# Performance work log

Hardware: AMD Instinct MI355X
Metric: run time of the kernel (lower is better)

## Reference

```python
import jax, jax.numpy as jnp
import numpy as np
from jax import lax

N, CIN, COUT, T, V = 32, 64, 128, 256, 25
IC = COUT // 4
EPS = 1e-5


def setup_inputs() -> dict:
    key = jax.random.key(0)
    ks = jax.random.split(key, 16)
    rn = lambda k, shape, s=0.05: jax.random.normal(k, shape, jnp.float32) * s
    inp = {
        'x': jax.random.normal(ks[0], (N, CIN, T, V), jnp.float32),
        'A': rn(ks[1], (V, V), 0.2),
        'w1': rn(ks[2], (IC, CIN)), 'b1': rn(ks[3], (IC,), 0.01),
        'w2': rn(ks[4], (IC, CIN)), 'b2': rn(ks[5], (IC,), 0.01),
        'w3': rn(ks[6], (COUT, CIN)), 'b3': rn(ks[7], (COUT,), 0.01),
        'w4': rn(ks[8], (COUT, CIN)), 'b4': rn(ks[9], (COUT,), 0.01),
        'bn1_g': jnp.ones((COUT,)), 'bn1_b': jnp.zeros((COUT,)),
        'bn1_m': rn(ks[10], (COUT,), 0.1), 'bn1_v': jnp.ones((COUT,)),
        'wt': rn(ks[11], (COUT, COUT, 9, 1)), 'bt': rn(ks[12], (COUT,), 0.01),
        'bn2_g': jnp.ones((COUT,)), 'bn2_b': jnp.zeros((COUT,)),
        'bn2_m': rn(ks[13], (COUT,), 0.1), 'bn2_v': jnp.ones((COUT,)),
        'wr': rn(ks[14], (COUT, CIN)), 'br': rn(ks[15], (COUT,), 0.01),
        'bnr_g': jnp.ones((COUT,)), 'bnr_b': jnp.zeros((COUT,)),
        'bnr_m': jnp.zeros((COUT,)), 'bnr_v': jnp.ones((COUT,)),
    }
    return inp


def _conv1x1(x, w, b):
    # 1x1 Conv2d over (T,V): pure channel mix. x: [N,C,T,V], w: [O,C]
    return jnp.einsum('oc,nctv->notv', w, x) + b[None, :, None, None]


def _bn(x, g, b, m, v):
    # BatchNorm2d in eval mode (running stats)
    scale = g / jnp.sqrt(v + EPS)
    return x * scale[None, :, None, None] + (b - m * scale)[None, :, None, None]


def _forward(x, A, w1, b1, w2, b2, w3, b3, w4, b4,
             bn1_g, bn1_b, bn1_m, bn1_v, wt, bt,
             bn2_g, bn2_b, bn2_m, bn2_v, wr, br,
             bnr_g, bnr_b, bnr_m, bnr_v):
    n, _, t, v = x.shape
    cout = w3.shape[0]
    ic = cout // 4
    x1 = _conv1x1(x, w1, b1).mean(axis=2)  # [N,IC,V]
    x2 = _conv1x1(x, w2, b2).mean(axis=2)  # [N,IC,V]
    a = jax.nn.softmax(x1[..., :, None] - x2[..., None, :], axis=-1)  # [N,IC,V,V]
    x3 = _conv1x1(x, w3, b3).reshape(n, 4, ic, t, v)
    y = jnp.einsum('ncuv,nmctv->nmctu', a, x3).reshape(n, cout, t, v)
    y = y + jnp.einsum('uv,nctv->nctu', A, _conv1x1(x, w4, b4))
    # tcn: BN -> ReLU -> Conv2d (9,1) pad (4,0) -> BN
    y = jax.nn.relu(_bn(y, bn1_g, bn1_b, bn1_m, bn1_v))
    y = lax.conv_general_dilated(
        y, wt, window_strides=(1, 1), padding=[(4, 4), (0, 0)],
        dimension_numbers=('NCHW', 'OIHW', 'NCHW')) + bt[None, :, None, None]
    y = _bn(y, bn2_g, bn2_b, bn2_m, bn2_v)
    # residual branch (in_channels != out_channels): 1x1 conv + BN
    res = _bn(_conv1x1(x, wr, br), bnr_g, bnr_b, bnr_m, bnr_v)
    return jax.nn.relu(y + res)


def reference(x, A, w1, b1, w2, b2, w3, b3, w4, b4,
              bn1_g, bn1_b, bn1_m, bn1_v, wt, bt,
              bn2_g, bn2_b, bn2_m, bn2_v, wr, br,
              bnr_g, bnr_b, bnr_m, bnr_v):
    return _forward(x, A, w1, b1, w2, b2, w3, b3, w4, b4,
                    bn1_g, bn1_b, bn1_m, bn1_v, wt, bt,
                    bn2_g, bn2_b, bn2_m, bn2_v, wr, br,
                    bnr_g, bnr_b, bnr_m, bnr_v)
```

## Files before the change

### kernel.cpp

```cpp
#include <hip/hip_runtime.h>
#include <hip/hip_bf16.h>

typedef unsigned short u16;
typedef unsigned int u32;
typedef unsigned long long u64;
typedef __attribute__((ext_vector_type(8))) short short8;
typedef __attribute__((ext_vector_type(4))) float f32x4;

#define DI __device__ __forceinline__

DI float b2f(u16 v){ u32 u = ((u32)v) << 16; float f; __builtin_memcpy(&f, &u, 4); return f; }
DI u16 f2bu(float f){ __hip_bfloat16 h = __float2bfloat16(f); u16 u; __builtin_memcpy(&u, &h, 2); return u; }

DI void gll16(const u16* g, u16* l){
  __builtin_amdgcn_global_load_lds((const __attribute__((address_space(1))) void*)g,
                                   (__attribute__((address_space(3))) void*)l, 16, 0, 0);
}

__global__ __launch_bounds__(256) void kaux(const float* __restrict__ wt, const float* __restrict__ wrw,
      const float* __restrict__ g2, const float* __restrict__ v2,
      const float* __restrict__ gr, const float* __restrict__ vr,
      const float* __restrict__ w3, const float* __restrict__ w4,
      const float* __restrict__ bt, const float* __restrict__ bb2, const float* __restrict__ m2,
      const float* __restrict__ bbr, const float* __restrict__ mr, const float* __restrict__ brb,
      float* __restrict__ xm, u16* __restrict__ wtb, u16* __restrict__ wrb,
      u16* __restrict__ w3b, u16* __restrict__ w4b,
      float* __restrict__ e0, float* __restrict__ e1, u16* __restrict__ h){
  const int b = blockIdx.x, tid = threadIdx.x;
  if (b < 50){
    const int i = b*1024 + tid*4;
    float4 z = {0.f,0.f,0.f,0.f};
    *(float4*)(xm + i) = z;
  } else if (b < 626){
    const int o = (b-50)*256 + tid;
    const int dt = o >> 14, rem = o & 16383;
    wtb[o] = f2bu(wt[rem*9 + dt]);
  } else if (b < 658){
    const int o = (b-626)*256 + tid;
    const int co = o >> 6;
    const float E0 = g2[co]*rsqrtf(v2[co]+1e-5f);
    const float R0 = gr[co]*rsqrtf(vr[co]+1e-5f);
    wrb[o] = f2bu(wrw[o]*R0/E0);
  } else if (b < 690){
    const int o = (b-658)*256 + tid;
    w3b[o] = f2bu(w3[o]);
  } else if (b < 722){
    const int o = (b-690)*256 + tid;
    w4b[o] = f2bu(w4[o]);
  } else if (b < 786){
    const int j = b - 722, n = j >> 1, side = j & 1;
    short8* base = (short8*)(h + ((size_t)n*6600 + (side ? 6500 : 0))*128);
    short8 z = {0,0,0,0,0,0,0,0};
    for (int i = tid; i < 1600; i += 256) base[i] = z;
  } else {
    if (tid < 128){
      const float scv2 = g2[tid]*rsqrtf(v2[tid]+1e-5f);
      const float scvr = gr[tid]*rsqrtf(vr[tid]+1e-5f);
      e0[tid] = scv2;
      e1[tid] = scv2*bt[tid] + bb2[tid] - m2[tid]*scv2
              + (bbr[tid] - mr[tid]*scvr + scvr*brb[tid]);
    }
  }
}

__global__ __launch_bounds__(256) void kprep2(const float* __restrict__ x, const float* __restrict__ Ab,
                                              u16* __restrict__ xT, u16* __restrict__ xA){
  __shared__ float xl[200*68];
  __shared__ float al[625];
  const int tc = blockIdx.x, n = blockIdx.y, tid = threadIdx.x;
  const int x0t = tc * 200;
  for (int i = tid; i < 625; i += 256) al[i] = Ab[i];
  for (int idx = tid; idx < 12800; idx += 256){
    const int ci = idx / 200, col = idx - ci*200;
    xl[col*68 + ci] = x[((size_t)(n*64+ci))*6400 + x0t + col];
  }
  __syncthreads();
  for (int idx = tid; idx < 3200; idx += 256){
    const int r = idx >> 4, k4 = (idx & 15) << 2;
    const float* src = xl + r*68 + k4;
    u64 pk = (u64)f2bu(src[0]) | ((u64)f2bu(src[1])<<16)
           | ((u64)f2bu(src[2])<<32) | ((u64)f2bu(src[3])<<48);
    *(u64*)(xT + ((size_t)n*6400 + x0t + r)*64 + k4) = pk;
  }
  if (tid < 200){
    const int t_ = tid / 25, u = tid % 25;
    float acc[64];
    #pragma unroll
    for (int k = 0; k < 64; k++) acc[k] = 0.f;
    const float* arow = al + u*25;
    for (int v = 0; v < 25; v++){
      const float a = arow[v];
      const float* xr = xl + (t_*25 + v)*68;
      #pragma unroll
      for (int k = 0; k < 64; k++) acc[k] += a * xr[k];
    }
    u16* dst = xA + ((size_t)n*6400 + x0t + tid)*64;
    #pragma unroll
    for (int k = 0; k < 64; k += 4){
      u64 pk = (u64)f2bu(acc[k]) | ((u64)f2bu(acc[k+1])<<16)
             | ((u64)f2bu(acc[k+2])<<32) | ((u64)f2bu(acc[k+3])<<48);
      *(u64*)(dst + k) = pk;
    }
  }
}

__global__ __launch_bounds__(256) void kmean(const u16* __restrict__ xT, float* __restrict__ xm){
  __shared__ float part[4][1600];
  const int seg = blockIdx.x, n = blockIdx.y, tid = threadIdx.x;
  const int tg = tid>>6, c = tid&63;
  float acc[25];
  #pragma unroll
  for (int v=0;v<25;v++) acc[v]=0.f;
  for (int t = seg*32 + tg; t < seg*32 + 32; t += 4){
    const u16* base = xT + ((size_t)n*6400 + t*25)*64 + c;
    #pragma unroll
    for (int v=0;v<25;v++) acc[v] += b2f(base[v*64]);
  }
  #pragma unroll
  for (int v=0;v<25;v++) part[tg][v*64+c] = acc[v];
  __syncthreads();
  for (int idx = tid; idx < 1600; idx += 256){
    const int v = idx>>6, cc = idx&63;
    const float m = part[0][idx]+part[1][idx]+part[2][idx]+part[3][idx];
    atomicAdd(&xm[(n*64+cc)*25+v], m*(1.f/256.f));
  }
}

__global__ __launch_bounds__(64) void kp(const float* __restrict__ xm, const float* __restrict__ w2,
                                         const float* __restrict__ b2p, const float* __restrict__ Ab,
                                         float* __restrict__ p, float* __restrict__ rsA){
  const int c = blockIdx.x, n = blockIdx.y, lane = threadIdx.x;
  __shared__ float sc[32];
  __shared__ float red[2];
  float neg = 0.f;
  if (lane < 25){
    float acc = b2p[c];
    for (int k = 0; k < 64; k++) acc += w2[c*64 + k] * xm[(n*64 + k)*25 + lane];
    neg = -acc;
    sc[lane] = neg;
  }
  __syncthreads();
  if (lane == 0){
    float m = sc[0];
    for (int i = 1; i < 25; i++) m = fmaxf(m, sc[i]);
    red[0] = m;
  }
  __syncthreads();
  float e = 0.f;
  if (lane < 25){ e = expf(neg - red[0]); sc[lane] = e; }
  __syncthreads();
  if (lane == 0){
    float ssum = 0.f;
    for (int i = 0; i < 25; i++) ssum += sc[i];
    red[1] = ssum;
  }
  __syncthreads();
  if (lane < 25) p[(n*32 + c)*25 + lane] = e / red[1];
  if (n == 0 && c == 0 && lane < 25){
    float r = 0.f;
    for (int v = 0; v < 25; v++) r += Ab[lane*25 + v];
    rsA[lane] = r;
  }
}

__global__ __launch_bounds__(256) void ks(const u16* __restrict__ xT, const u16* __restrict__ w3b,
                                          const float* __restrict__ p, float* __restrict__ s){
  __shared__ __align__(16) char smem[53248];
  __shared__ float pL[800];
  u16* aL = (u16*)smem;
  u16* bL = (u16*)(smem + 18432);
  float* z3 = (float*)smem;
  const int xb = blockIdx.x, n = blockIdx.y, tid = threadIdx.x;
  const int x0 = xb*100, t0 = xb*4;
  const int row = tid >> 1, half = tid & 1;
  {
    short8* dst = (short8*)(aL + row*72 + half*32);
    const short8* src = (const short8*)(w3b + row*64 + half*32);
    #pragma unroll
    for (int i=0;i<4;i++) dst[i] = src[i];
  }
  {
    short8* dst = (short8*)(bL + row*72 + half*32);
    if (row < 100){
      const short8* src = (const short8*)(xT + ((size_t)n*6400 + x0 + row)*64 + half*32);
      #pragma unroll
      for (int i=0;i<4;i++) dst[i] = src[i];
    } else {
      short8 z = {0,0,0,0,0,0,0,0};
      #pragma unroll
      for (int i=0;i<4;i++) dst[i] = z;
    }
  }
  for (int i = tid; i < 800; i += 256) pL[i] = p[n*800 + i];
  __syncthreads();
  const int wave = tid>>6, lane = tid&63, q = lane>>4, l = lane&15;
  const int wr = wave>>1, wc = wave&1;
  f32x4 acc[4][4];
  #pragma unroll
  for (int i=0;i<4;i++)
    #pragma unroll
    for (int j=0;j<4;j++){ f32x4 z0 = {0.f,0.f,0.f,0.f}; acc[i][j] = z0; }
  #pragma unroll
  for (int ksi = 0; ksi < 2; ksi++){
    const int kb = ksi*32 + q*8;
    short8 af[4], bf[4];
    #pragma unroll
    for (int i=0;i<4;i++) af[i] = *(const short8*)(aL + (wr*64 + i*16 + l)*72 + kb);
    #pragma unroll
    for (int j=0;j<4;j++) bf[j] = *(const short8*)(bL + (wc*64 + j*16 + l)*72 + kb);
    #pragma unroll
    for (int i=0;i<4;i++)
      #pragma unroll
      for (int j=0;j<4;j++)
        acc[i][j] = __builtin_amdgcn_mfma_f32_16x16x32_bf16(af[i], bf[j], acc[i][j], 0, 0, 0);
  }
  __syncthreads();
  #pragma unroll
  for (int i=0;i<4;i++){
    const int co0 = wr*64 + i*16 + q*4;
    #pragma unroll
    for (int j=0;j<4;j++){
      const int colx = wc*64 + j*16 + l;
      if (colx < 100){
        #pragma unroll
        for (int r=0;r<4;r++) z3[(co0 + r)*104 + colx] = acc[i][j][r];
      }
    }
  }
  __syncthreads();
  for (int idx = tid; idx < 512; idx += 256){
    const int co = idx >> 2, tt = idx & 3;
    const float* zr = z3 + co*104 + tt*25;
    const float* pr = pL + (co & 31)*25;
    float acc2 = 0.f;
    #pragma unroll
    for (int v=0; v<25; v++) acc2 += zr[v]*pr[v];
    s[((size_t)n*128 + co)*256 + t0 + tt] = acc2;
  }
}

__global__ __launch_bounds__(256) void ky(const u16* __restrict__ xA, const u16* __restrict__ w4b,
      const float* __restrict__ s, const float* __restrict__ b3, const float* __restrict__ b4,
      const float* __restrict__ g1, const float* __restrict__ bb1, const float* __restrict__ m1,
      const float* __restrict__ v1, const float* __restrict__ rsA, u16* __restrict__ h){
  __shared__ __align__(16) u16 aL[128*72];
  __shared__ __align__(16) u16 bL[128*72];
  __shared__ float A0[128], A1[128], A2[128];
  __shared__ float sF[1024];
  __shared__ float rs[32];
  const int xb = blockIdx.x, n = blockIdx.y, tid = threadIdx.x;
  const int x0 = xb*128, tlo = x0/25;
  const int row = tid >> 1, half = tid & 1;
  {
    short8* dst = (short8*)(aL + row*72 + half*32);
    const short8* src = (const short8*)(w4b + row*64 + half*32);
    #pragma unroll
    for (int i=0;i<4;i++) dst[i] = src[i];
  }
  {
    const short8* src = (const short8*)(xA + ((size_t)n*6400 + x0 + row)*64 + half*32);
    short8* dst = (short8*)(bL + row*72 + half*32);
    #pragma unroll
    for (int i=0;i<4;i++) dst[i] = src[i];
  }
  if (tid < 128){
    const float scv = g1[tid] * rsqrtf(v1[tid] + 1e-5f);
    A0[tid] = scv;
    A1[tid] = scv * b4[tid];
    A2[tid] = bb1[tid] - m1[tid] * scv;
  }
  if (tid < 32) rs[tid] = (tid < 25) ? rsA[tid] : 0.f;
  __syncthreads();
  for (int idx = tid; idx < 1024; idx += 256){
    const int co = idx >> 3, tt = idx & 7;
    const int t = tlo + tt;
    const float sv = (t < 256) ? s[((size_t)n*128 + co)*256 + t] : 0.f;
    sF[idx] = A0[co] * (sv + b3[co]) + A2[co];
  }
  const int wave = tid>>6, lane = tid&63, q = lane>>4, l = lane&15;
  const int wr = wave>>1, wc = wave&1;
  f32x4 acc[4][4];
  #pragma unroll
  for (int i=0;i<4;i++)
    #pragma unroll
    for (int j=0;j<4;j++){ f32x4 z0 = {0.f,0.f,0.f,0.f}; acc[i][j] = z0; }
  #pragma unroll
  for (int ksi = 0; ksi < 2; ksi++){
    const int kb = ksi*32 + q*8;
    short8 af[4], bf[4];
    #pragma unroll
    for (int i=0;i<4;i++) af[i] = *(const short8*)(aL + (wr*64 + i*16 + l)*72 + kb);
    #pragma unroll
    for (int j=0;j<4;j++) bf[j] = *(const short8*)(bL + (wc*64 + j*16 + l)*72 + kb);
    #pragma unroll
    for (int i=0;i<4;i++)
      #pragma unroll
      for (int j=0;j<4;j++)
        acc[i][j] = __builtin_amdgcn_mfma_f32_16x16x32_bf16(af[i], bf[j], acc[i][j], 0, 0, 0);
  }
  __syncthreads();
  #pragma unroll
  for (int i=0;i<4;i++){
    const int co0 = wr*64 + i*16 + q*4;
    #pragma unroll
    for (int j=0;j<4;j++){
      const int colx = wc*64 + j*16 + l;
      const int xg = x0 + colx;
      const int u = xg % 25, tt = xg/25 - tlo;
      const float rsu = rs[u];
      u64 pk = 0;
      #pragma unroll
      for (int r=0;r<4;r++){
        const int co = co0 + r;
        float y = A0[co]*acc[i][j][r] + A1[co]*rsu + sF[co*8 + tt];
        y = fmaxf(y, 0.f);
        pk |= ((u64)f2bu(y)) << (16*r);
      }
      *(u64*)(h + ((size_t)n*6600 + xg + 100)*128 + co0) = pk;
    }
  }
}

__global__ __launch_bounds__(512, 2) void ktcn(const u16* __restrict__ h, const u16* __restrict__ wtb,
      const u16* __restrict__ wrb, const u16* __restrict__ xT,
      const float* __restrict__ e0g, const float* __restrict__ e1g,
      float* __restrict__ out){
  __shared__ __align__(16) char smem[149504];
  u16* hW = (u16*)smem;
  u16* Ab0 = (u16*)(smem + 83968);
  u16* Ab1 = (u16*)(smem + 116736);
  const int xb = blockIdx.x, n = blockIdx.y, tid = threadIdx.x;
  const int x0 = xb*128;
  const int wave = tid>>6, lane = tid&63, q = lane>>4, l = lane&15;
  const int wr2 = wave>>2, wc = wave&3;
  const u16* hbase = h + ((size_t)n*6600 + x0)*128;
  const u16* xtb = xT + ((size_t)n*6400 + x0)*64;

  f32x4 e0r[4], e1r[4];
  #pragma unroll
  for (int i=0;i<4;i++){
    const int co0 = wr2*64 + i*16 + q*4;
    e0r[i] = *(const f32x4*)(e0g + co0);
    e1r[i] = *(const f32x4*)(e1g + co0);
  }

  #pragma unroll
  for (int it = 0; it < 4; ++it){
    const int ci = it*512 + tid;
    const int r = ci >> 4, c = ci & 15;
    gll16(hbase + r*128 + ((c ^ (r & 15))<<3), hW + ((it*512 + wave*64)<<3));
  }
  #pragma unroll
  for (int it = 0; it < 4; ++it){
    const int ci = it*512 + tid;
    const int r = ci >> 4, c = ci & 15;
    gll16(wtb + r*128 + ((c ^ (r & 15))<<3), Ab0 + ((it*512 + wave*64)<<3));
  }
  #pragma unroll
  for (int it = 0; it < 4; ++it){
    const int ci = it*512 + tid;
    const int r = ci >> 4, c = ci & 15;
    gll16(wtb + 16384 + r*128 + ((c ^ (r & 15))<<3), Ab1 + ((it*512 + wave*64)<<3));
  }
  #pragma unroll
  for (int it = 4; it < 6; ++it){
    const int ci = it*512 + tid;
    const int r = ci >> 4, c = ci & 15;
    gll16(hbase + r*128 + ((c ^ (r & 15))<<3), hW + ((it*512 + wave*64)<<3));
  }

  f32x4 acc[4][2];
  #pragma unroll
  for (int i=0;i<4;i++)
    #pragma unroll
    for (int j=0;j<2;j++){ f32x4 z0 = {0.f,0.f,0.f,0.f}; acc[i][j] = z0; }

  asm volatile("s_waitcnt vmcnt(6) lgkmcnt(0)" ::: "memory");
  __builtin_amdgcn_s_barrier();
  __builtin_amdgcn_sched_barrier(0);

  #pragma unroll 1
  for (int dt = 0; dt <= 9; ++dt){
    if (dt >= 1 && dt <= 7){
      const u16* gA = wtb + (dt+1)*16384;
      u16* dA = ((dt+1) & 1) ? Ab1 : Ab0;
      #pragma unroll
      for (int it = 0; it < 4; ++it){
        const int ci = it*512 + tid;
        const int r = ci >> 4, c = ci & 15;
        gll16(gA + r*128 + ((c ^ (r & 15))<<3), dA + ((it*512 + wave*64)<<3));
      }
    } else if (dt == 8){
      #pragma unroll
      for (int it = 0; it < 2; ++it){
        const int ci = it*512 + tid;
        const int r = ci >> 3, c = ci & 7;
        gll16(wrb + r*64 + ((c ^ (r & 7))<<3), Ab1 + ((it*512 + wave*64)<<3));
      }
      #pragma unroll
      for (int it = 0; it < 2; ++it){
        const int ci = it*512 + tid;
        const int r = ci >> 3, c = ci & 7;
        gll16(xtb + r*64 + ((c ^ (r & 7))<<3), Ab1 + 8192 + ((it*512 + wave*64)<<3));
      }
    }
    if (dt >= 1 && dt <= 4){
      const int it = 5 + dt;
      const int ci = it*512 + tid;
      const int r = ci >> 4, c = ci & 15;
      gll16(hbase + r*128 + ((c ^ (r & 15))<<3), hW + ((it*512 + wave*64)<<3));
      if (dt == 4 && tid < 128){
        const int ci2 = 5120 + tid;
        const int r2 = ci2 >> 4, c2 = ci2 & 15;
        gll16(hbase + r2*128 + ((c2 ^ (r2 & 15))<<3), hW + ((5120 + wave*64)<<3));
      }
    }
    if (dt < 9){
      const u16* A = (dt & 1) ? Ab1 : Ab0;
      #pragma unroll
      for (int ksi = 0; ksi < 4; ksi++){
        const int c0 = ksi*4 + q;
        short8 af[4], bf[2];
        #pragma unroll
        for (int i=0;i<4;i++){
          const int r = wr2*64 + i*16 + l;
          af[i] = *(const short8*)(A + (((r<<4) + (c0 ^ (r & 15)))<<3));
        }
        #pragma unroll
        for (int j=0;j<2;j++){
          const int r = dt*25 + wc*32 + j*16 + l;
          bf[j] = *(const short8*)(hW + (((r<<4) + (c0 ^ (r & 15)))<<3));
        }
        #pragma unroll
        for (int i=0;i<4;i++)
          #pragma unroll
          for (int j=0;j<2;j++)
            acc[i][j] = __builtin_amdgcn_mfma_f32_16x16x32_bf16(af[i], bf[j], acc[i][j], 0, 0, 0);
      }
    } else {
      const u16* A = Ab1;
      const u16* B = Ab1 + 8192;
      #pragma unroll
      for (int ksi = 0; ksi < 2; ksi++){
        const int c0 = ksi*4 + q;
        short8 af[4], bf[2];
        #pragma unroll
        for (int i=0;i<4;i++){
          const int r = wr2*64 + i*16 + l;
          af[i] = *(const short8*)(A + (((r<<3) + (c0 ^ (r & 7)))<<3));
        }
        #pragma unroll
        for (int j=0;j<2;j++){
          const int r = wc*32 + j*16 + l;
          bf[j] = *(const short8*)(B + (((r<<3) + (c0 ^ (r & 7)))<<3));
        }
        #pragma unroll
        for (int i=0;i<4;i++)
          #pragma unroll
          for (int j=0;j<2;j++)
            acc[i][j] = __builtin_amdgcn_mfma_f32_16x16x32_bf16(af[i], bf[j], acc[i][j], 0, 0, 0);
      }
    }
    if (dt < 9){
      if (dt <= 4){
        asm volatile("s_waitcnt vmcnt(1) lgkmcnt(0)" ::: "memory");
        __builtin_amdgcn_s_barrier();
        __builtin_amdgcn_sched_barrier(0);
      } else {
        __syncthreads();
      }
    }
  }

  #pragma unroll
  for (int i=0;i<4;i++){
    const int co0 = wr2*64 + i*16 + q*4;
    #pragma unroll
    for (int j=0;j<2;j++){
      const int colx = wc*32 + j*16 + l;
      #pragma unroll
      for (int r=0;r<4;r++){
        const float yv = e0r[i][r]*acc[i][j][r] + e1r[i][r];
        out[((size_t)n*128 + co0 + r)*6400 + x0 + colx] = fmaxf(yv, 0.f);
      }
    }
  }
}

extern "C" void kernel_launch(void* const* d_in, const int* in_sizes, int n_in,
                              void* d_out, int out_size, void* d_ws, size_t ws_size,
                              hipStream_t stream){
  const float* x   = (const float*)d_in[0];
  const float* Ab  = (const float*)d_in[1];
  const float* w2  = (const float*)d_in[4];
  const float* b2p = (const float*)d_in[5];
  const float* w3  = (const float*)d_in[6];
  const float* b3  = (const float*)d_in[7];
  const float* w4  = (const float*)d_in[8];
  const float* b4  = (const float*)d_in[9];
  const float* g1  = (const float*)d_in[10];
  const float* bb1 = (const float*)d_in[11];
  const float* m1  = (const float*)d_in[12];
  const float* v1  = (const float*)d_in[13];
  const float* wt  = (const float*)d_in[14];
  const float* bt  = (const float*)d_in[15];
  const float* g2  = (const float*)d_in[16];
  const float* bb2 = (const float*)d_in[17];
  const float* m2  = (const float*)d_in[18];
  const float* v2  = (const float*)d_in[19];
  const float* wrw = (const float*)d_in[20];
  const float* brb = (const float*)d_in[21];
  const float* gr  = (const float*)d_in[22];
  const float* bbr = (const float*)d_in[23];
  const float* mr  = (const float*)d_in[24];
  const float* vr  = (const float*)d_in[25];
  float* out = (float*)d_out;

  char* ws = (char*)d_ws;
  float* xm  = (float*)(ws);
  float* p   = (float*)(ws + 204800);
  float* rsA = (float*)(ws + 307200);
  float* s   = (float*)(ws + 307712);
  u16* xT    = (u16*)(ws + 4502016);
  u16* xA    = (u16*)(ws + 30716416);
  u16* h     = (u16*)(ws + 56930816);
  u16* wtb   = (u16*)(ws + 110998016);
  u16* wrb   = (u16*)(ws + 111292928);
  u16* w3b   = (u16*)(ws + 111309312);
  u16* w4b   = (u16*)(ws + 111325696);
  float* e0  = (float*)(ws + 111342080);
  float* e1  = (float*)(ws + 111342592);

  kaux<<<787, 256, 0, stream>>>(wt, wrw, g2, v2, gr, vr, w3, w4, bt, bb2, m2, bbr, mr, brb,
                                xm, wtb, wrb, w3b, w4b, e0, e1, h);
  kprep2<<<dim3(32,32), 256, 0, stream>>>(x, Ab, xT, xA);
  kmean<<<dim3(8,32), 256, 0, stream>>>(xT, xm);
  kp<<<dim3(32,32), 64, 0, stream>>>(xm, w2, b2p, Ab, p, rsA);
  ks<<<dim3(64,32), 256, 0, stream>>>(xT, w3b, p, s);
  ky<<<dim3(50,32), 256, 0, stream>>>(xA, w4b, s, b3, b4, g1, bb1, m1, v1, rsA, h);
  ktcn<<<dim3(50,32), 512, 0, stream>>>(h, wtb, wrb, xT, e0, e1, out);
}
```

Measured before the change: 397.8 us.

## Split K across wave pairs in ktcn with LDS reduction; vectorize x loads in kprep2

The ktcn main GEMM now gives each wave a 64x64 output tile over half of the K dimension, instead of a 64x32 tile over the full K. Paired waves combine their partial sums through LDS before the fused BN/ReLU epilogue. This raises MFMA work per fragment load, cutting LDS reads per MFMA, but doubles accumulator registers and adds a reduction barrier. Separately, kprep2 reads x with float4 global loads instead of scalar loads when transposing into LDS.

```diff
diff --git a/kernel.cpp b/kernel.cpp
--- a/kernel.cpp
+++ b/kernel.cpp
@@ -70,9 +70,11 @@
   const int tc = blockIdx.x, n = blockIdx.y, tid = threadIdx.x;
   const int x0t = tc * 200;
   for (int i = tid; i < 625; i += 256) al[i] = Ab[i];
-  for (int idx = tid; idx < 12800; idx += 256){
-    const int ci = idx / 200, col = idx - ci*200;
-    xl[col*68 + ci] = x[((size_t)(n*64+ci))*6400 + x0t + col];
+  for (int idx = tid; idx < 3200; idx += 256){
+    const int ci = idx / 50, c4 = idx - ci*50;
+    const float4 f = *(const float4*)(x + ((size_t)(n*64+ci))*6400 + x0t + c4*4);
+    float* d = xl + (c4*4)*68 + ci;
+    d[0] = f.x; d[68] = f.y; d[136] = f.z; d[204] = f.w;
   }
   __syncthreads();
   for (int idx = tid; idx < 3200; idx += 256){
@@ -329,10 +331,11 @@
   u16* hW = (u16*)smem;
   u16* Ab0 = (u16*)(smem + 83968);
   u16* Ab1 = (u16*)(smem + 116736);
+  float* red = (float*)smem;
   const int xb = blockIdx.x, n = blockIdx.y, tid = threadIdx.x;
   const int x0 = xb*128;
   const int wave = tid>>6, lane = tid&63, q = lane>>4, l = lane&15;
-  const int wr2 = wave>>2, wc = wave&3;
+  const int wr2 = (wave>>2)&1, wc2 = (wave>>1)&1, kh = wave&1;
   const u16* hbase = h + ((size_t)n*6600 + x0)*128;
   const u16* xtb = xT + ((size_t)n*6400 + x0)*64;
 
@@ -369,11 +372,11 @@
     gll16(hbase + r*128 + ((c ^ (r & 15))<<3), hW + ((it*512 + wave*64)<<3));
   }
 
-  f32x4 acc[4][2];
+  f32x4 acc[4][4];
   #pragma unroll
   for (int i=0;i<4;i++)
     #pragma unroll
-    for (int j=0;j<2;j++){ f32x4 z0 = {0.f,0.f,0.f,0.f}; acc[i][j] = z0; }
+    for (int j=0;j<4;j++){ f32x4 z0 = {0.f,0.f,0.f,0.f}; acc[i][j] = z0; }
 
   asm volatile("s_waitcnt vmcnt(6) lgkmcnt(0)" ::: "memory");
   __builtin_amdgcn_s_barrier();
@@ -418,48 +421,45 @@
     if (dt < 9){
       const u16* A = (dt & 1) ? Ab1 : Ab0;
       #pragma unroll
-      for (int ksi = 0; ksi < 4; ksi++){
-        const int c0 = ksi*4 + q;
-        short8 af[4], bf[2];
+      for (int ks2 = 0; ks2 < 2; ks2++){
+        const int c0 = (kh*2 + ks2)*4 + q;
+        short8 af[4], bf[4];
         #pragma unroll
         for (int i=0;i<4;i++){
           const int r = wr2*64 + i*16 + l;
           af[i] = *(const short8*)(A + (((r<<4) + (c0 ^ (r & 15)))<<3));
         }
         #pragma unroll
-        for (int j=0;j<2;j++){
-          const int r = dt*25 + wc*32 + j*16 + l;
+        for (int j=0;j<4;j++){
+          const int r = dt*25 + wc2*64 + j*16 + l;
           bf[j] = *(const short8*)(hW + (((r<<4) + (c0 ^ (r & 15)))<<3));
         }
         #pragma unroll
         for (int i=0;i<4;i++)
           #pragma unroll
-          for (int j=0;j<2;j++)
+          for (int j=0;j<4;j++)
             acc[i][j] = __builtin_amdgcn_mfma_f32_16x16x32_bf16(af[i], bf[j], acc[i][j], 0, 0, 0);
       }
     } else {
       const u16* A = Ab1;
       const u16* B = Ab1 + 8192;
-      #pragma unroll
-      for (int ksi = 0; ksi < 2; ksi++){
-        const int c0 = ksi*4 + q;
-        short8 af[4], bf[2];
-        #pragma unroll
-        for (int i=0;i<4;i++){
-          const int r = wr2*64 + i*16 + l;
-          af[i] = *(const short8*)(A + (((r<<3) + (c0 ^ (r & 7)))<<3));
-        }
-        #pragma unroll
-        for (int j=0;j<2;j++){
-          const int r = wc*32 + j*16 + l;
-          bf[j] = *(const short8*)(B + (((r<<3) + (c0 ^ (r & 7)))<<3));
-        }
-        #pragma unroll
-        for (int i=0;i<4;i++)
-          #pragma unroll
-          for (int j=0;j<2;j++)
-            acc[i][j] = __builtin_amdgcn_mfma_f32_16x16x32_bf16(af[i], bf[j], acc[i][j], 0, 0, 0);
-      }
+      const int c0 = kh*4 + q;
+      short8 af[4], bf[4];
+      #pragma unroll
+      for (int i=0;i<4;i++){
+        const int r = wr2*64 + i*16 + l;
+        af[i] = *(const short8*)(A + (((r<<3) + (c0 ^ (r & 7)))<<3));
+      }
+      #pragma unroll
+      for (int j=0;j<4;j++){
+        const int r = wc2*64 + j*16 + l;
+        bf[j] = *(const short8*)(B + (((r<<3) + (c0 ^ (r & 7)))<<3));
+      }
+      #pragma unroll
+      for (int i=0;i<4;i++)
+        #pragma unroll
+        for (int j=0;j<4;j++)
+          acc[i][j] = __builtin_amdgcn_mfma_f32_16x16x32_bf16(af[i], bf[j], acc[i][j], 0, 0, 0);
     }
     if (dt < 9){
       if (dt <= 4){
@@ -472,16 +472,31 @@
     }
   }
 
-  #pragma unroll
-  for (int i=0;i<4;i++){
-    const int co0 = wr2*64 + i*16 + q*4;
-    #pragma unroll
-    for (int j=0;j<2;j++){
-      const int colx = wc*32 + j*16 + l;
-      #pragma unroll
-      for (int r=0;r<4;r++){
-        const float yv = e0r[i][r]*acc[i][j][r] + e1r[i][r];
-        out[((size_t)n*128 + co0 + r)*6400 + x0 + colx] = fmaxf(yv, 0.f);
+  const int pos = wr2*2 + wc2;
+  float* rb = red + pos*4096;
+  if (kh == 1){
+    #pragma unroll
+    for (int i=0;i<4;i++)
+      #pragma unroll
+      for (int j=0;j<4;j++)
+        #pragma unroll
+        for (int r=0;r<4;r++)
+          rb[(i*16 + q*4 + r)*64 + j*16 + l] = acc[i][j][r];
+  }
+  __syncthreads();
+  if (kh == 0){
+    #pragma unroll
+    for (int i=0;i<4;i++){
+      const int co0 = wr2*64 + i*16 + q*4;
+      #pragma unroll
+      for (int j=0;j<4;j++){
+        const int colx = wc2*64 + j*16 + l;
+        #pragma unroll
+        for (int r=0;r<4;r++){
+          const float v = acc[i][j][r] + rb[(i*16 + q*4 + r)*64 + j*16 + l];
+          const float yv = e0r[i][r]*v + e1r[i][r];
+          out[((size_t)n*128 + co0 + r)*6400 + x0 + colx] = fmaxf(yv, 0.f);
+        }
       }
     }
   }
```

After: 401.7 us. No clear change (+1.0%).
